# Optimization experiments

Measured on AMD Instinct MI355X. Metric: run time of the kernel, lower is better.

The kernel has to match this reference:

```python
import jax, jax.numpy as jnp
import numpy as np

NEG = 10000.0

def setup_inputs() -> dict:
    key = jax.random.key(0)
    ks = jax.random.split(key, 5)
    B, S, D = 2, 2048, 1024
    std = 1.0 / np.sqrt(D)
    return {
        "x": jax.random.normal(ks[0], (B, S, D), dtype=jnp.float32),
        "Wq": jax.random.normal(ks[1], (D, D), dtype=jnp.float32) * std,
        "bq": jnp.zeros((D,), jnp.float32),
        "Wk": jax.random.normal(ks[2], (D, D), dtype=jnp.float32) * std,
        "bk": jnp.zeros((D,), jnp.float32),
        "Wv": jax.random.normal(ks[3], (D, D), dtype=jnp.float32) * std,
        "bv": jnp.zeros((D,), jnp.float32),
        "Wo": jax.random.normal(ks[4], (D, D), dtype=jnp.float32) * std,
        "bo": jnp.zeros((D,), jnp.float32),
    }

def reference(x, Wq, bq, Wk, bk, Wv, bv, Wo, bo):
    # Linear projections + relu activation (as in the keras layer; note: no head split
    # is performed in this implementation, head_num is only a divisibility check).
    q = jax.nn.relu(x @ Wq + bq)  # [B,S,D]
    k = jax.nn.relu(x @ Wk + bk)
    v = jax.nn.relu(x @ Wv + bv)
    D = q.shape[-1]
    e = jnp.einsum('bqd,bkd->bqk', q, k) / jnp.sqrt(jnp.float32(D))  # [B,S,S]
    # history_only causal mask: penalize key positions j > query position i
    S = e.shape[-1]
    causal = (jnp.arange(S)[None, :] > jnp.arange(S)[:, None]).astype(e.dtype)
    e = e - NEG * causal[None, :, :]
    # stable softmax exactly as in the source (max-subtract, exp, normalize)
    e = jnp.exp(e - jnp.max(e, axis=-1, keepdims=True))
    attn = e / jnp.sum(e, axis=-1, keepdims=True)
    y = jnp.einsum('bqk,bkd->bqd', attn, v)
    return jax.nn.relu(y @ Wo + bo)
```

## Files before the change

kernel.cpp:

```cpp
#include <hip/hip_runtime.h>
#include <math.h>


typedef _Float16 f16x8 __attribute__((ext_vector_type(8)));
typedef float f32x4 __attribute__((ext_vector_type(4)));

#define BK 32

__device__ __forceinline__ void gload_lds16(const void* g, void* l) {
  __builtin_amdgcn_global_load_lds(
      (const __attribute__((address_space(1))) void*)g,
      (__attribute__((address_space(3))) void*)l, 16, 0, 0);
}

template<int TMp, int TNp>
__device__ __forceinline__ void gemm_acc(
    const _Float16* __restrict__ A, const _Float16* __restrict__ BT,
    _Float16* Ah, _Float16* Bh, int sAr, int sBr, int kend, int m0, int n0,
    f32x4 (&acc)[TMp / 32][TNp / 32])
{
  const int tid  = threadIdx.x;
  const int lane = tid & 63;
  const int wid  = tid >> 6;
  const int wm   = (wid >> 1) * (TMp / 2);
  const int wn   = (wid & 1) * (TNp / 2);
  const int l15  = lane & 15;
  const int quad = lane >> 4;
  constexpr int MT = TMp / 32;
  constexpr int NT = TNp / 32;
  constexpr int AI = TMp / 64;
  constexpr int BI = TNp / 64;
  const int r16 = lane >> 2;
  const int swc = ((lane & 3) ^ ((lane >> 3) & 3)) * 8;
  const int arow = wid * (TMp / 4);
  const int brow = wid * (TNp / 4);

  for (int k0 = 0; k0 < kend; k0 += BK) {
    #pragma unroll
    for (int t = 0; t < AI; ++t)
      gload_lds16(A + (long long)(m0 + arow + t * 16 + r16) * sAr + k0 + swc,
                  Ah + (arow + t * 16) * BK);
    #pragma unroll
    for (int t = 0; t < BI; ++t)
      gload_lds16(BT + (long long)(n0 + brow + t * 16 + r16) * sBr + k0 + swc,
                  Bh + (brow + t * 16) * BK);
    __syncthreads();

    const int ch = (quad ^ ((l15 >> 1) & 3)) * 8;
    const _Float16* ab = Ah + (wm + l15) * BK + ch;
    const _Float16* bb = Bh + (wn + l15) * BK + ch;
    f16x8 af[MT], bf[NT];
    #pragma unroll
    for (int t = 0; t < MT; ++t) af[t] = *(const f16x8*)(ab + t * 16 * BK);
    #pragma unroll
    for (int t = 0; t < NT; ++t) bf[t] = *(const f16x8*)(bb + t * 16 * BK);
    #pragma unroll
    for (int mt = 0; mt < MT; ++mt)
      #pragma unroll
      for (int nt = 0; nt < NT; ++nt)
        acc[mt][nt] = __builtin_amdgcn_mfma_f32_16x16x32_f16(
            af[mt], bf[nt], acc[mt][nt], 0, 0, 0);
    __syncthreads();
  }
}

template<int TMp, int TNp, bool RELU, bool HAS_BIAS, typename OT>
__device__ __forceinline__ void gemm_store(
    f32x4 (&acc)[TMp / 32][TNp / 32], const float* __restrict__ bias,
    OT* __restrict__ C, int Nout, float scale, int m0, int n0)
{
  const int tid  = threadIdx.x;
  const int lane = tid & 63;
  const int wid  = tid >> 6;
  const int wm   = (wid >> 1) * (TMp / 2);
  const int wn   = (wid & 1) * (TNp / 2);
  const int l15  = lane & 15;
  const int quad = lane >> 4;
  constexpr int MT = TMp / 32;
  constexpr int NT = TNp / 32;

  float bvals[NT];
  if (HAS_BIAS) {
    #pragma unroll
    for (int nt = 0; nt < NT; ++nt)
      bvals[nt] = bias[n0 + wn + nt * 16 + l15];
  }
  #pragma unroll
  for (int mt = 0; mt < MT; ++mt) {
    #pragma unroll
    for (int nt = 0; nt < NT; ++nt) {
      const int col = n0 + wn + nt * 16 + l15;
      #pragma unroll
      for (int r = 0; r < 4; ++r) {
        const int row = m0 + wm + mt * 16 + quad * 4 + r;
        float v = acc[mt][nt][r] * scale;
        if (HAS_BIAS) v += bvals[nt];
        if (RELU) v = fmaxf(v, 0.f);
        C[(long long)row * Nout + col] = (OT)v;
      }
    }
  }
}

__global__ __launch_bounds__(256) void qkv_kernel(
    const _Float16* __restrict__ xh, const _Float16* __restrict__ Wcat,
    const float* __restrict__ bq, const float* __restrict__ bk,
    const float* __restrict__ bv,
    _Float16* __restrict__ Qh, _Float16* __restrict__ Kh,
    _Float16* __restrict__ Vh, int D)
{
  __shared__ _Float16 Ah[128 * BK];
  __shared__ _Float16 Bh[128 * BK];
  const int m0  = blockIdx.y * 128;
  const int n0g = blockIdx.x * 128;
  f32x4 acc[4][4];
  #pragma unroll
  for (int i = 0; i < 4; ++i)
    #pragma unroll
    for (int j = 0; j < 4; ++j) acc[i][j] = (f32x4){0.f, 0.f, 0.f, 0.f};

  gemm_acc<128, 128>(xh, Wcat, Ah, Bh, D, D, D, m0, n0g, acc);

  const int mat = n0g >> 10;
  const int c0  = n0g & 1023;
  _Float16* C = (mat == 0) ? Qh : (mat == 1) ? Kh : Vh;
  const float* bias = (mat == 0) ? bq : (mat == 1) ? bk : bv;
  gemm_store<128, 128, true, true, _Float16>(acc, bias, C, D, 1.0f, m0, c0);
}

__global__ __launch_bounds__(256) void mid_kernel(
    const _Float16* __restrict__ Qh, const _Float16* __restrict__ Kh,
    _Float16* __restrict__ E, const _Float16* __restrict__ WoT,
    const _Float16* __restrict__ Vh, _Float16* __restrict__ VWT,
    int S, int D)
{
  __shared__ _Float16 Ah[128 * BK];
  __shared__ _Float16 Bh[64 * BK];
  const _Float16 *A, *BT;
  _Float16* C;
  int m0, n0;
  float scale;
  const int id = blockIdx.x;
  if (id < 544) {
    const int z = (id >= 272);
    const int t = id - z * 272;
    int i = (int)((sqrtf(4.f * t + 1.f) - 1.f) * 0.5f);
    while ((i + 1) * (i + 2) <= t) ++i;
    while (i * (i + 1) > t) --i;
    const int j = t - i * (i + 1);
    m0 = i * 128;
    n0 = j * 64;
    A  = Qh + (long long)z * S * D;
    BT = Kh + (long long)z * S * D;
    C  = E + (long long)z * S * S;
    scale = 0.03125f;
  } else {
    const int t = id - 544;
    const int z = t >> 8;
    const int u = t & 255;
    m0 = (u >> 5) * 128;
    n0 = (u & 31) * 64;
    A  = WoT;
    BT = Vh + (long long)z * S * D;
    C  = VWT + (long long)z * D * S;
    scale = 1.0f;
  }
  f32x4 acc[4][2];
  #pragma unroll
  for (int i = 0; i < 4; ++i)
    #pragma unroll
    for (int j = 0; j < 2; ++j) acc[i][j] = (f32x4){0.f, 0.f, 0.f, 0.f};

  gemm_acc<128, 64>(A, BT, Ah, Bh, D, D, D, m0, n0, acc);
  gemm_store<128, 64, false, false, _Float16>(acc, nullptr, C, S, scale, m0, n0);
}

__global__ __launch_bounds__(256) void pv_kernel(
    const _Float16* __restrict__ E, const _Float16* __restrict__ VWT,
    const float* __restrict__ bo, float* __restrict__ out, int S, int D)
{
  __shared__ _Float16 Ah[64 * BK];
  __shared__ _Float16 Bh[128 * BK];
  const int z  = blockIdx.z;
  const int m0 = ((int)gridDim.y - 1 - (int)blockIdx.y) * 64;
  const int n0 = blockIdx.x * 128;
  const _Float16* A  = E + (long long)z * S * S;
  const _Float16* BT = VWT + (long long)z * D * S;
  float* C = out + (long long)z * S * D;
  const int kend = m0 + 64;

  f32x4 acc[2][4];
  #pragma unroll
  for (int i = 0; i < 2; ++i)
    #pragma unroll
    for (int j = 0; j < 4; ++j) acc[i][j] = (f32x4){0.f, 0.f, 0.f, 0.f};

  gemm_acc<64, 128>(A, BT, Ah, Bh, S, S, kend, m0, n0, acc);
  gemm_store<64, 128, true, true, float>(acc, bo, C, D, 1.0f, m0, n0);
}

__global__ __launch_bounds__(256) void prep_kernel(
    const float* __restrict__ x, _Float16* __restrict__ xh,
    const float* __restrict__ W0, const float* __restrict__ W1,
    const float* __restrict__ W2, const float* __restrict__ W3,
    _Float16* __restrict__ Wcat, int D)
{
  const int id = blockIdx.x;
  const int tid = threadIdx.x;
  if (id < 2048) {
    const long long i = ((long long)id * 256 + tid) * 8;
    float4 a = *(const float4*)(x + i);
    float4 b = *(const float4*)(x + i + 4);
    f16x8 o = {(_Float16)a.x, (_Float16)a.y, (_Float16)a.z, (_Float16)a.w,
               (_Float16)b.x, (_Float16)b.y, (_Float16)b.z, (_Float16)b.w};
    *(f16x8*)(xh + i) = o;
    return;
  }
  __shared__ _Float16 t[64][72];
  const int u = id - 2048;
  const int z = u >> 8;
  const int v = u & 255;
  const float* W = (z == 0) ? W0 : (z == 1) ? W1 : (z == 2) ? W2 : W3;
  _Float16* dst = Wcat + (long long)z * D * D;
  const int k0 = (v >> 4) * 64, n0 = (v & 15) * 64;
  #pragma unroll
  for (int it = 0; it < 4; ++it) {
    int idx = tid + it * 256;
    int r = idx >> 4, c4 = (idx & 15) << 2;
    float4 w = *(const float4*)(W + (long long)(k0 + r) * D + n0 + c4);
    t[r][c4 + 0] = (_Float16)w.x; t[r][c4 + 1] = (_Float16)w.y;
    t[r][c4 + 2] = (_Float16)w.z; t[r][c4 + 3] = (_Float16)w.w;
  }
  __syncthreads();
  #pragma unroll
  for (int it = 0; it < 2; ++it) {
    int idx = tid + it * 256;
    int r = idx >> 3, c8 = (idx & 7) << 3;
    f16x8 o;
    #pragma unroll
    for (int j = 0; j < 8; ++j) o[j] = t[c8 + j][r];
    *(f16x8*)(dst + (long long)(n0 + r) * D + k0 + c8) = o;
  }
}

__global__ __launch_bounds__(256) void softmax_causal_h(
    _Float16* __restrict__ E, int S)
{
  const int i = blockIdx.x;
  _Float16* row = E + ((long long)blockIdx.y * S + i) * S;
  const int tid = threadIdx.x;
  const int n = i + 1;
  const int j0 = tid * 8;

  f16x8 hv = *(const f16x8*)(row + j0);
  float vals[8];
  float m = -3.0e38f;
  #pragma unroll
  for (int t = 0; t < 8; ++t) {
    float v = (j0 + t < n) ? (float)hv[t] : -3.0e38f;
    vals[t] = v;
    m = fmaxf(m, v);
  }
  #pragma unroll
  for (int o = 32; o > 0; o >>= 1) m = fmaxf(m, __shfl_down(m, o, 64));

  __shared__ float rmax[4];
  __shared__ float rsum[4];
  const int wave = tid >> 6;
  if ((tid & 63) == 0) rmax[wave] = m;
  __syncthreads();
  m = fmaxf(fmaxf(rmax[0], rmax[1]), fmaxf(rmax[2], rmax[3]));

  float s = 0.f;
  #pragma unroll
  for (int t = 0; t < 8; ++t) {
    float e = (j0 + t < n) ? expf(vals[t] - m) : 0.f;
    vals[t] = e;
    s += e;
  }
  #pragma unroll
  for (int o = 32; o > 0; o >>= 1) s += __shfl_down(s, o, 64);
  if ((tid & 63) == 0) rsum[wave] = s;
  __syncthreads();
  s = rsum[0] + rsum[1] + rsum[2] + rsum[3];

  const float inv = 1.0f / s;
  f16x8 ov;
  #pragma unroll
  for (int t = 0; t < 8; ++t) ov[t] = (_Float16)(vals[t] * inv);
  *(f16x8*)(row + j0) = ov;
}

extern "C" void kernel_launch(void* const* d_in, const int* in_sizes, int n_in,
                              void* d_out, int out_size, void* d_ws, size_t ws_size,
                              hipStream_t stream) {
  const float* x  = (const float*)d_in[0];
  const float* Wq = (const float*)d_in[1];
  const float* bq = (const float*)d_in[2];
  const float* Wk = (const float*)d_in[3];
  const float* bk = (const float*)d_in[4];
  const float* Wv = (const float*)d_in[5];
  const float* bv = (const float*)d_in[6];
  const float* Wo = (const float*)d_in[7];
  const float* bo = (const float*)d_in[8];
  float* out = (float*)d_out;

  const int Bn = 2, S = 2048, D = 1024;
  const int M = Bn * S;
  const size_t MD = (size_t)M * D;
  const size_t DD = (size_t)D * D;
  const size_t SS = (size_t)Bn * S * S;

  _Float16* ws   = (_Float16*)d_ws;
  _Float16* xh   = ws;
  _Float16* Wcat = xh + MD;
  _Float16* Qh   = Wcat + 4 * DD;
  _Float16* Kh   = Qh + MD;
  _Float16* Vh   = Kh + MD;
  _Float16* VWT  = Vh + MD;
  _Float16* E    = VWT + MD;

  dim3 blk(256);

  prep_kernel<<<dim3(3072), blk, 0, stream>>>(x, xh, Wq, Wk, Wv, Wo, Wcat, D);

  qkv_kernel<<<dim3(3 * D / 128, M / 128), blk, 0, stream>>>(
      xh, Wcat, bq, bk, bv, Qh, Kh, Vh, D);

  mid_kernel<<<dim3(1056), blk, 0, stream>>>(
      Qh, Kh, E, Wcat + 3 * DD, Vh, VWT, S, D);

  softmax_causal_h<<<dim3(S, Bn), blk, 0, stream>>>(E, S);

  pv_kernel<<<dim3(D / 128, S / 64, Bn), blk, 0, stream>>>(
      E, VWT, bo, out, S, D);
}
```

Baseline: 208.8 us.

## Fuse causal softmax into PV GEMM with masked score stores

Removes the separate softmax kernel. The score GEMM now writes a large negative value into masked causal positions, and the PV kernel computes each row's max and sum by re-reading the raw scores before its main loop. The exponential and normalisation are applied on the fly to the A fragments inside the MFMA loop. This saves one kernel launch and a full read-write pass over the score matrix, at the cost of an extra read pass per row and redundant exp work repeated across the eight column blocks of the output.

```diff
diff --git a/kernel.cpp b/kernel.cpp
--- a/kernel.cpp
+++ b/kernel.cpp
@@ -64,7 +64,7 @@
   }
 }
 
-template<int TMp, int TNp, bool RELU, bool HAS_BIAS, typename OT>
+template<int TMp, int TNp, bool RELU, bool HAS_BIAS, bool CMASK, typename OT>
 __device__ __forceinline__ void gemm_store(
     f32x4 (&acc)[TMp / 32][TNp / 32], const float* __restrict__ bias,
     OT* __restrict__ C, int Nout, float scale, int m0, int n0)
@@ -96,6 +96,7 @@
         float v = acc[mt][nt][r] * scale;
         if (HAS_BIAS) v += bvals[nt];
         if (RELU) v = fmaxf(v, 0.f);
+        if (CMASK && col > row) v = -3000.0f;
         C[(long long)row * Nout + col] = (OT)v;
       }
     }
@@ -125,7 +126,7 @@
   const int c0  = n0g & 1023;
   _Float16* C = (mat == 0) ? Qh : (mat == 1) ? Kh : Vh;
   const float* bias = (mat == 0) ? bq : (mat == 1) ? bk : bv;
-  gemm_store<128, 128, true, true, _Float16>(acc, bias, C, D, 1.0f, m0, c0);
+  gemm_store<128, 128, true, true, false, _Float16>(acc, bias, C, D, 1.0f, m0, c0);
 }
 
 __global__ __launch_bounds__(256) void mid_kernel(
@@ -136,11 +137,13 @@
 {
   __shared__ _Float16 Ah[128 * BK];
   __shared__ _Float16 Bh[64 * BK];
-  const _Float16 *A, *BT;
-  _Float16* C;
-  int m0, n0;
-  float scale;
   const int id = blockIdx.x;
+  f32x4 acc[4][2];
+  #pragma unroll
+  for (int i = 0; i < 4; ++i)
+    #pragma unroll
+    for (int j = 0; j < 2; ++j) acc[i][j] = (f32x4){0.f, 0.f, 0.f, 0.f};
+
   if (id < 544) {
     const int z = (id >= 272);
     const int t = id - z * 272;
@@ -148,31 +151,22 @@
     while ((i + 1) * (i + 2) <= t) ++i;
     while (i * (i + 1) > t) --i;
     const int j = t - i * (i + 1);
-    m0 = i * 128;
-    n0 = j * 64;
-    A  = Qh + (long long)z * S * D;
-    BT = Kh + (long long)z * S * D;
-    C  = E + (long long)z * S * S;
-    scale = 0.03125f;
+    const int m0 = i * 128, n0 = j * 64;
+    gemm_acc<128, 64>(Qh + (long long)z * S * D, Kh + (long long)z * S * D,
+                      Ah, Bh, D, D, D, m0, n0, acc);
+    gemm_store<128, 64, false, false, true, _Float16>(
+        acc, nullptr, E + (long long)z * S * S, S, 0.03125f, m0, n0);
   } else {
     const int t = id - 544;
     const int z = t >> 8;
     const int u = t & 255;
-    m0 = (u >> 5) * 128;
-    n0 = (u & 31) * 64;
-    A  = WoT;
-    BT = Vh + (long long)z * S * D;
-    C  = VWT + (long long)z * D * S;
-    scale = 1.0f;
-  }
-  f32x4 acc[4][2];
-  #pragma unroll
-  for (int i = 0; i < 4; ++i)
-    #pragma unroll
-    for (int j = 0; j < 2; ++j) acc[i][j] = (f32x4){0.f, 0.f, 0.f, 0.f};
-
-  gemm_acc<128, 64>(A, BT, Ah, Bh, D, D, D, m0, n0, acc);
-  gemm_store<128, 64, false, false, _Float16>(acc, nullptr, C, S, scale, m0, n0);
+    const int m0 = (u >> 5) * 128;
+    const int n0 = (u & 31) * 64;
+    gemm_acc<128, 64>(WoT, Vh + (long long)z * S * D,
+                      Ah, Bh, D, D, D, m0, n0, acc);
+    gemm_store<128, 64, false, false, false, _Float16>(
+        acc, nullptr, VWT + (long long)z * D * S, S, 1.0f, m0, n0);
+  }
 }
 
 __global__ __launch_bounds__(256) void pv_kernel(
@@ -181,22 +175,101 @@
 {
   __shared__ _Float16 Ah[64 * BK];
   __shared__ _Float16 Bh[128 * BK];
+  __shared__ float rowinfo[128];
   const int z  = blockIdx.z;
   const int m0 = ((int)gridDim.y - 1 - (int)blockIdx.y) * 64;
   const int n0 = blockIdx.x * 128;
-  const _Float16* A  = E + (long long)z * S * S;
+  const _Float16* Eb = E + (long long)z * S * S;
   const _Float16* BT = VWT + (long long)z * D * S;
   float* C = out + (long long)z * S * D;
   const int kend = m0 + 64;
 
+  const int tid = threadIdx.x;
+  {
+    const int r = tid >> 2;
+    const int c = tid & 3;
+    const _Float16* rowp = Eb + (long long)(m0 + r) * S;
+    float mx = -3.0e38f;
+    for (int j = c * 8; j < kend; j += 32) {
+      f16x8 v = *(const f16x8*)(rowp + j);
+      #pragma unroll
+      for (int t = 0; t < 8; ++t) mx = fmaxf(mx, (float)v[t]);
+    }
+    mx = fmaxf(mx, __shfl_xor(mx, 1, 64));
+    mx = fmaxf(mx, __shfl_xor(mx, 2, 64));
+    float sm = 0.f;
+    for (int j = c * 8; j < kend; j += 32) {
+      f16x8 v = *(const f16x8*)(rowp + j);
+      #pragma unroll
+      for (int t = 0; t < 8; ++t) sm += __expf((float)v[t] - mx);
+    }
+    sm += __shfl_xor(sm, 1, 64);
+    sm += __shfl_xor(sm, 2, 64);
+    if (c == 0) { rowinfo[r * 2] = mx; rowinfo[r * 2 + 1] = 1.0f / sm; }
+  }
+  __syncthreads();
+
+  const int lane = tid & 63;
+  const int wid  = tid >> 6;
+  const int wm   = (wid >> 1) * 32;
+  const int wn   = (wid & 1) * 64;
+  const int l15  = lane & 15;
+  const int quad = lane >> 4;
+
+  float mrow[2], il[2];
+  #pragma unroll
+  for (int mt = 0; mt < 2; ++mt) {
+    const int rl = wm + mt * 16 + l15;
+    mrow[mt] = rowinfo[rl * 2];
+    il[mt]   = rowinfo[rl * 2 + 1];
+  }
+
   f32x4 acc[2][4];
   #pragma unroll
-  for (int i = 0; i < 2; ++i)
-    #pragma unroll
-    for (int j = 0; j < 4; ++j) acc[i][j] = (f32x4){0.f, 0.f, 0.f, 0.f};
-
-  gemm_acc<64, 128>(A, BT, Ah, Bh, S, S, kend, m0, n0, acc);
-  gemm_store<64, 128, true, true, float>(acc, bo, C, D, 1.0f, m0, n0);
+  for (int a = 0; a < 2; ++a)
+    #pragma unroll
+    for (int b = 0; b < 4; ++b) acc[a][b] = (f32x4){0.f, 0.f, 0.f, 0.f};
+
+  const int r16 = lane >> 2;
+  const int swc = ((lane & 3) ^ ((lane >> 3) & 3)) * 8;
+  const int arow = wid * 16;
+  const int brow = wid * 32;
+
+  for (int k0 = 0; k0 < kend; k0 += BK) {
+    gload_lds16(Eb + (long long)(m0 + arow + r16) * S + k0 + swc,
+                Ah + arow * BK);
+    #pragma unroll
+    for (int t = 0; t < 2; ++t)
+      gload_lds16(BT + (long long)(n0 + brow + t * 16 + r16) * S + k0 + swc,
+                  Bh + (brow + t * 16) * BK);
+    __syncthreads();
+
+    const int ch = (quad ^ ((l15 >> 1) & 3)) * 8;
+    const _Float16* ab = Ah + (wm + l15) * BK + ch;
+    const _Float16* bb = Bh + (wn + l15) * BK + ch;
+    f16x8 af[2], bf[4];
+    #pragma unroll
+    for (int t = 0; t < 2; ++t) af[t] = *(const f16x8*)(ab + t * 16 * BK);
+    #pragma unroll
+    for (int mt = 0; mt < 2; ++mt) {
+      f16x8 p;
+      #pragma unroll
+      for (int e = 0; e < 8; ++e)
+        p[e] = (_Float16)(__expf((float)af[mt][e] - mrow[mt]) * il[mt]);
+      af[mt] = p;
+    }
+    #pragma unroll
+    for (int t = 0; t < 4; ++t) bf[t] = *(const f16x8*)(bb + t * 16 * BK);
+    #pragma unroll
+    for (int mt = 0; mt < 2; ++mt)
+      #pragma unroll
+      for (int nt = 0; nt < 4; ++nt)
+        acc[mt][nt] = __builtin_amdgcn_mfma_f32_16x16x32_f16(
+            af[mt], bf[nt], acc[mt][nt], 0, 0, 0);
+    __syncthreads();
+  }
+
+  gemm_store<64, 128, true, true, false, float>(acc, bo, C, D, 1.0f, m0, n0);
 }
 
 __global__ __launch_bounds__(256) void prep_kernel(
@@ -241,54 +314,6 @@
     for (int j = 0; j < 8; ++j) o[j] = t[c8 + j][r];
     *(f16x8*)(dst + (long long)(n0 + r) * D + k0 + c8) = o;
   }
-}
-
-__global__ __launch_bounds__(256) void softmax_causal_h(
-    _Float16* __restrict__ E, int S)
-{
-  const int i = blockIdx.x;
-  _Float16* row = E + ((long long)blockIdx.y * S + i) * S;
-  const int tid = threadIdx.x;
-  const int n = i + 1;
-  const int j0 = tid * 8;
-
-  f16x8 hv = *(const f16x8*)(row + j0);
-  float vals[8];
-  float m = -3.0e38f;
-  #pragma unroll
-  for (int t = 0; t < 8; ++t) {
-    float v = (j0 + t < n) ? (float)hv[t] : -3.0e38f;
-    vals[t] = v;
-    m = fmaxf(m, v);
-  }
-  #pragma unroll
-  for (int o = 32; o > 0; o >>= 1) m = fmaxf(m, __shfl_down(m, o, 64));
-
-  __shared__ float rmax[4];
-  __shared__ float rsum[4];
-  const int wave = tid >> 6;
-  if ((tid & 63) == 0) rmax[wave] = m;
-  __syncthreads();
-  m = fmaxf(fmaxf(rmax[0], rmax[1]), fmaxf(rmax[2], rmax[3]));
-
-  float s = 0.f;
-  #pragma unroll
-  for (int t = 0; t < 8; ++t) {
-    float e = (j0 + t < n) ? expf(vals[t] - m) : 0.f;
-    vals[t] = e;
-    s += e;
-  }
-  #pragma unroll
-  for (int o = 32; o > 0; o >>= 1) s += __shfl_down(s, o, 64);
-  if ((tid & 63) == 0) rsum[wave] = s;
-  __syncthreads();
-  s = rsum[0] + rsum[1] + rsum[2] + rsum[3];
-
-  const float inv = 1.0f / s;
-  f16x8 ov;
-  #pragma unroll
-  for (int t = 0; t < 8; ++t) ov[t] = (_Float16)(vals[t] * inv);
-  *(f16x8*)(row + j0) = ov;
 }
 
 extern "C" void kernel_launch(void* const* d_in, const int* in_sizes, int n_in,
@@ -330,8 +355,6 @@
   mid_kernel<<<dim3(1056), blk, 0, stream>>>(
       Qh, Kh, E, Wcat + 3 * DD, Vh, VWT, S, D);
 
-  softmax_causal_h<<<dim3(S, Bn), blk, 0, stream>>>(E, S);
-
   pv_kernel<<<dim3(D / 128, S / 64, Bn), blk, 0, stream>>>(
       E, VWT, bo, out, S, D);
 }
```

Measured after the change: 269.8 us. 1.29x slower.
